# Optimization experiments

Hardware: AMD Instinct MI355X
Metric: run time of the kernel (lower is better)

The kernel has to match this reference:

```python
import jax, jax.numpy as jnp
import numpy as np

D = 1024; NHEAD = 8; NQ = 256; B = 8; HM = 64; WM = 64; S = HM * WM; FF = 4 * D
EPS_LN = 1e-5


def _ln(x, g, b):
    m = x.mean(-1, keepdims=True)
    v = ((x - m) ** 2).mean(-1, keepdims=True)
    return (x - m) / jnp.sqrt(v + EPS_LN) * g + b


def _self_attn(x, w_in, b_in, w_out, b_out, nhead):
    # x: [L, B, D] (torch MultiheadAttention, batch_first=False, eval mode)
    L, Bn, Dm = x.shape
    hd = Dm // nhead
    qkv = x @ w_in.T + b_in  # [L, B, 3D]
    q, k, v = jnp.split(qkv, 3, axis=-1)
    sp = lambda t: t.reshape(L, Bn, nhead, hd).transpose(1, 2, 0, 3)  # [B, H, L, hd]
    q, k, v = sp(q), sp(k), sp(v)
    attn = jax.nn.softmax(jnp.einsum('bhqd,bhkd->bhqk', q, k) / float(hd) ** 0.5, axis=-1)
    out = jnp.einsum('bhqk,bhkd->bhqd', attn, v)
    out = out.transpose(2, 0, 1, 3).reshape(L, Bn, Dm)
    return out @ w_out.T + b_out


def setup_inputs() -> dict:
    key = jax.random.key(0)
    ks = iter(jax.random.split(key, 40))
    nrm = lambda shape: jax.random.normal(next(ks), shape, jnp.float32) * 0.02
    return dict(
        query=jax.random.normal(next(ks), (NQ, B, D), jnp.float32),
        memory=jax.random.normal(next(ks), (S, B, D), jnp.float32),
        prev_mask=jax.random.uniform(next(ks), (B, NQ, HM, WM), dtype=jnp.float32),
        h_mem=HM, w_mem=WM,
        sa_in_w=nrm((3 * D, D)), sa_in_b=jnp.zeros((3 * D,), jnp.float32),
        sa_out_w=nrm((D, D)), sa_out_b=jnp.zeros((D,), jnp.float32),
        ln1_g=jnp.ones((D,), jnp.float32), ln1_b=jnp.zeros((D,), jnp.float32),
        ln2_g=jnp.ones((D,), jnp.float32), ln2_b=jnp.zeros((D,), jnp.float32),
        ln3_g=jnp.ones((D,), jnp.float32), ln3_b=jnp.zeros((D,), jnp.float32),
        wq=nrm((D, D)), bq=jnp.zeros((D,), jnp.float32),
        wk=nrm((D, D)), bk=jnp.zeros((D,), jnp.float32),
        wv=nrm((D, D)), bv=jnp.zeros((D,), jnp.float32),
        wo=nrm((D, D)), bo=jnp.zeros((D,), jnp.float32),
        w1=nrm((FF, D)), b1=jnp.zeros((FF,), jnp.float32),
        w2=nrm((D, FF)), b2=jnp.zeros((D,), jnp.float32),
        mask_w=nrm((S, D)), mask_b=jnp.zeros((S,), jnp.float32),
    )


def reference(query, memory, prev_mask, h_mem, w_mem,
              sa_in_w, sa_in_b, sa_out_w, sa_out_b,
              ln1_g, ln1_b, ln2_g, ln2_b, ln3_g, ln3_b,
              wq, bq, wk, bk, wv, bv, wo, bo,
              w1, b1, w2, b2, mask_w, mask_b):
    nq, Bn, d_model = query.shape
    # --- self attention block ---
    q_norm = _ln(query, ln1_g, ln1_b)
    q2 = _self_attn(q_norm, sa_in_w, sa_in_b, sa_out_w, sa_out_b, NHEAD)
    query = query + q2
    # --- masked cross attention (single-head, as in source) ---
    Q = (_ln(query, ln2_g, ln2_b) @ wq.T + bq).transpose(1, 0, 2)  # [B, NQ, D]
    K = (memory @ wk.T + bk).transpose(1, 0, 2)                    # [B, S, D]
    V = (memory @ wv.T + bv).transpose(1, 0, 2)                    # [B, S, D]
    scores = jnp.einsum('bqd,bsd->bqs', Q, K) / float(d_model) ** 0.5
    scores = scores + jnp.log(prev_mask.reshape(Bn, nq, -1) + 1e-6)
    attn = jax.nn.softmax(scores, axis=-1)
    attn_out = jnp.einsum('bqs,bsd->bqd', attn, V).transpose(1, 0, 2)  # [NQ, B, D]
    query = query + (attn_out @ wo.T + bo)
    # --- FFN ---
    h = jax.nn.gelu(_ln(query, ln3_g, ln3_b) @ w1.T + b1, approximate=False)
    query = query + (h @ w2.T + b2)
    # --- mask prediction ---
    q_for_mask = query.transpose(1, 0, 2)                # [B, NQ, D]
    mask_logits = q_for_mask @ mask_w.T + mask_b          # [B, NQ, H*W]
    pred_mask = jax.nn.sigmoid(mask_logits.reshape(Bn, nq, h_mem, w_mem))
    return (query, pred_mask)
```

## Files before the change

### kernel.cpp

```cpp
#include <hip/hip_runtime.h>
#include <cstdint>


typedef __attribute__((ext_vector_type(8))) __bf16 bf16x8;
typedef __attribute__((ext_vector_type(4))) float f32x4;
typedef __attribute__((ext_vector_type(8))) unsigned short ushort8;
typedef __attribute__((ext_vector_type(4))) unsigned short ushort4v;

__device__ __forceinline__ unsigned short f2bf(float f) {
  return __builtin_bit_cast(unsigned short, (__bf16)f);
}

__global__ __launch_bounds__(256) void cast_bf16_kernel(const float* __restrict__ in,
                                                        unsigned short* __restrict__ out,
                                                        int n8) {
  int i = blockIdx.x * 256 + threadIdx.x;
  if (i >= n8) return;
  const float4* p = (const float4*)in + (size_t)i * 2;
  float4 a = p[0], b = p[1];
  ushort8 o;
  o[0] = f2bf(a.x); o[1] = f2bf(a.y); o[2] = f2bf(a.z); o[3] = f2bf(a.w);
  o[4] = f2bf(b.x); o[5] = f2bf(b.y); o[6] = f2bf(b.z); o[7] = f2bf(b.w);
  ((ushort8*)out)[i] = o;
}

struct CastSegs {
  const float* src[9];
  int cum[10];
};
__global__ __launch_bounds__(256) void cast_multi_kernel(CastSegs cs,
                                                         unsigned short* __restrict__ out) {
  int i = blockIdx.x * 256 + threadIdx.x;
  if (i >= cs.cum[9]) return;
  int s = 0;
  while (i >= cs.cum[s + 1]) s++;
  const float4* p = (const float4*)cs.src[s] + (size_t)(i - cs.cum[s]) * 2;
  float4 a = p[0], b = p[1];
  ushort8 o;
  o[0] = f2bf(a.x); o[1] = f2bf(a.y); o[2] = f2bf(a.z); o[3] = f2bf(a.w);
  o[4] = f2bf(b.x); o[5] = f2bf(b.y); o[6] = f2bf(b.z); o[7] = f2bf(b.w);
  ((ushort8*)out)[i] = o;
}

__global__ __launch_bounds__(256) void bias_concat_kernel(const float* __restrict__ a,
                                                          const float* __restrict__ b,
                                                          float* __restrict__ o) {
  int i = blockIdx.x * 256 + threadIdx.x;
  o[i] = i < 1024 ? a[i] : b[i - 1024];
}

__global__ __launch_bounds__(256) void ln_bf16_kernel(const float* __restrict__ x,
                                                      const float* __restrict__ g,
                                                      const float* __restrict__ b,
                                                      unsigned short* __restrict__ out) {
  int row = blockIdx.x, tid = threadIdx.x;
  const float4* xr = (const float4*)(x + (size_t)row * 1024);
  float4 v = xr[tid];
  float s = v.x + v.y + v.z + v.w;
  float sq = v.x * v.x + v.y * v.y + v.z * v.z + v.w * v.w;
#pragma unroll
  for (int o = 32; o > 0; o >>= 1) { s += __shfl_xor(s, o); sq += __shfl_xor(sq, o); }
  __shared__ float red[8];
  int wave = tid >> 6, lane = tid & 63;
  if (lane == 0) { red[wave] = s; red[4 + wave] = sq; }
  __syncthreads();
  float ts = red[0] + red[1] + red[2] + red[3];
  float tq = red[4] + red[5] + red[6] + red[7];
  float mean = ts * (1.f / 1024.f);
  float var = tq * (1.f / 1024.f) - mean * mean;
  float rstd = rsqrtf(var + 1e-5f);
  float4 gv = ((const float4*)g)[tid];
  float4 bv = ((const float4*)b)[tid];
  ushort4v o;
  o[0] = f2bf((v.x - mean) * rstd * gv.x + bv.x);
  o[1] = f2bf((v.y - mean) * rstd * gv.y + bv.y);
  o[2] = f2bf((v.z - mean) * rstd * gv.z + bv.z);
  o[3] = f2bf((v.w - mean) * rstd * gv.w + bv.w);
  ((ushort4v*)(out + (size_t)row * 1024))[tid] = o;
}

template <bool MASK, int CNT>
__global__ __launch_bounds__(256) void softmax_bf16_kernel(const float* __restrict__ sc,
                                                           const float* __restrict__ pm,
                                                           unsigned short* __restrict__ out,
                                                           float scale) {
  const int L = CNT * 256;
  int row = blockIdx.x, tid = threadIdx.x;
  const float* sr = sc + (size_t)row * L;
  float vals[CNT];
  float mx = -1e30f;
#pragma unroll
  for (int i = 0; i < CNT; i++) {
    int idx = tid + (i << 8);
    float v = sr[idx] * scale;
    if (MASK) v += __logf(pm[(size_t)row * L + idx] + 1e-6f);
    vals[i] = v;
    mx = fmaxf(mx, v);
  }
#pragma unroll
  for (int o = 32; o > 0; o >>= 1) mx = fmaxf(mx, __shfl_xor(mx, o));
  __shared__ float red[8];
  int wave = tid >> 6, lane = tid & 63;
  if (lane == 0) red[wave] = mx;
  __syncthreads();
  mx = fmaxf(fmaxf(red[0], red[1]), fmaxf(red[2], red[3]));
  float sum = 0.f;
#pragma unroll
  for (int i = 0; i < CNT; i++) { vals[i] = __expf(vals[i] - mx); sum += vals[i]; }
#pragma unroll
  for (int o = 32; o > 0; o >>= 1) sum += __shfl_xor(sum, o);
  if (lane == 0) red[4 + wave] = sum;
  __syncthreads();
  float rs = 1.f / (red[4] + red[5] + red[6] + red[7]);
#pragma unroll
  for (int i = 0; i < CNT; i++)
    out[(size_t)row * L + tid + (i << 8)] = f2bf(vals[i] * rs);
}

__global__ __launch_bounds__(256) void transpose_bf16_kernel(
    const unsigned short* __restrict__ in, unsigned short* __restrict__ out,
    long in_off, int in_rs, long in_hi, long in_lo, int zdiv,
    long out_off, int out_rs, long out_hi, long out_lo) {
  __shared__ unsigned short t[32][33];
  int z = blockIdx.z;
  int zh = z / zdiv, zl = z % zdiv;
  const unsigned short* ib = in + in_off + (long)zh * in_hi + (long)zl * in_lo;
  unsigned short* ob = out + out_off + (long)zh * out_hi + (long)zl * out_lo;
  int i0 = blockIdx.x * 32;
  int j0 = blockIdx.y * 32;
  int tx = threadIdx.x & 31, ty = threadIdx.x >> 5;
#pragma unroll
  for (int r = ty; r < 32; r += 8) t[r][tx] = ib[(long)(j0 + r) * in_rs + i0 + tx];
  __syncthreads();
#pragma unroll
  for (int r = ty; r < 32; r += 8) ob[(long)(i0 + r) * out_rs + j0 + tx] = t[tx][r];
}

template <int TM, bool AF32, bool BIAS, int ACT, bool RES, bool OUTF, bool OUTB, bool KVSPLIT>
__global__ __launch_bounds__(256) void gemm_nt_kernel(
    const void* __restrict__ Av, long a_off, int lda, long a_hi, long a_lo,
    const unsigned short* __restrict__ B, long b_off, int ldb, long b_hi, long b_lo,
    const float* __restrict__ bias, const float* __restrict__ Res,
    float* __restrict__ Cf, long c_off, int ldc, long c_hi, long c_lo,
    unsigned short* __restrict__ Cb, long cb_off, int ldcb, long cb_hi, long cb_lo,
    int K, int zdiv) {
  constexpr int MI = TM / 32;
  __shared__ unsigned short As[2 * TM * 32];
  __shared__ unsigned short Bs[2 * 128 * 32];
  int tid = threadIdx.x;
  int wave = tid >> 6, lane = tid & 63;
  int z = blockIdx.z, zh = z / zdiv, zl = z % zdiv;
  long m0 = (long)blockIdx.x * TM, n0 = (long)blockIdx.y * 128;

  const unsigned short* Bb = B + b_off + zh * b_hi + zl * b_lo + n0 * ldb;
  const unsigned short* Ab16 = nullptr;
  const float* Abf = nullptr;
  if constexpr (AF32)
    Abf = (const float*)Av + a_off + zh * a_hi + zl * a_lo + m0 * lda;
  else
    Ab16 = (const unsigned short*)Av + a_off + zh * a_hi + zl * a_lo + m0 * lda;

  int srow = lane >> 2;
  int scol = (lane & 3) * 8;
  int wm = (wave >> 1) * (TM / 2), wn = (wave & 1) * 64;
  int fr = lane & 15;
  int ko = (lane >> 4) * 8;

  f32x4 acc[MI][4] = {};

  auto stage = [&](int buf, int k0) {
    unsigned short* Ad = As + buf * (TM * 32);
    unsigned short* Bd = Bs + buf * (128 * 32);
    if constexpr (AF32) {
      int row = tid >> 1;
      int cs = (tid & 1) * 16;
      const float* ap = Abf + (long)row * lda + k0 + cs;
      float4 f0 = ((const float4*)ap)[0];
      float4 f1 = ((const float4*)ap)[1];
      float4 f2 = ((const float4*)ap)[2];
      float4 f3 = ((const float4*)ap)[3];
      ushort8 u0, u1;
      u0[0] = f2bf(f0.x); u0[1] = f2bf(f0.y); u0[2] = f2bf(f0.z); u0[3] = f2bf(f0.w);
      u0[4] = f2bf(f1.x); u0[5] = f2bf(f1.y); u0[6] = f2bf(f1.z); u0[7] = f2bf(f1.w);
      u1[0] = f2bf(f2.x); u1[1] = f2bf(f2.y); u1[2] = f2bf(f2.z); u1[3] = f2bf(f2.w);
      u1[4] = f2bf(f3.x); u1[5] = f2bf(f3.y); u1[6] = f2bf(f3.z); u1[7] = f2bf(f3.w);
      ushort8* dst = (ushort8*)(Ad + row * 32 + cs);
      dst[0] = u0;
      dst[1] = u1;
    } else {
#pragma unroll
      for (int is = 0; is < TM / 64; is++) {
        int rbase = wave * (TM / 4) + is * 16;
        const unsigned short* g = Ab16 + (long)(rbase + srow) * lda + k0 + scol;
        __builtin_amdgcn_global_load_lds(
            (const __attribute__((address_space(1))) unsigned int*)g,
            (__attribute__((address_space(3))) unsigned int*)(Ad + rbase * 32), 16, 0, 0);
      }
    }
#pragma unroll
    for (int is = 0; is < 2; is++) {
      int rbase = wave * 32 + is * 16;
      const unsigned short* g = Bb + (long)(rbase + srow) * ldb + k0 + scol;
      __builtin_amdgcn_global_load_lds(
          (const __attribute__((address_space(1))) unsigned int*)g,
          (__attribute__((address_space(3))) unsigned int*)(Bd + rbase * 32), 16, 0, 0);
    }
  };

  stage(0, 0);
  int cur = 0;
  for (int k0 = 0; k0 < K; k0 += 32, cur ^= 1) {
    __syncthreads();
    if (k0 + 32 < K) stage(cur ^ 1, k0 + 32);

    const unsigned short* Ar = As + cur * (TM * 32);
    const unsigned short* Br = Bs + cur * (128 * 32);
    bf16x8 af[MI], bfv[4];
#pragma unroll
    for (int i = 0; i < MI; i++)
      af[i] = *(const bf16x8*)(Ar + (wm + i * 16 + fr) * 32 + ko);
#pragma unroll
    for (int j = 0; j < 4; j++)
      bfv[j] = *(const bf16x8*)(Br + (wn + j * 16 + fr) * 32 + ko);
#pragma unroll
    for (int i = 0; i < MI; i++)
#pragma unroll
      for (int j = 0; j < 4; j++)
        acc[i][j] = __builtin_amdgcn_mfma_f32_16x16x32_bf16(af[i], bfv[j], acc[i][j], 0, 0, 0);
  }

  long cfo = c_off + zh * c_hi + zl * c_lo;
  long cbo = cb_off + zh * cb_hi + zl * cb_lo;
  int rq = (lane >> 4) * 4;
#pragma unroll
  for (int i = 0; i < MI; i++) {
    long rbase = m0 + wm + i * 16 + rq;
#pragma unroll
    for (int j = 0; j < 4; j++) {
      long cc = n0 + wn + j * 16 + fr;
      float bsv = BIAS ? bias[cc] : 0.f;
      long p = KVSPLIT ? ((cc >> 10) * cb_hi + (cc & 1023)) : cc;
#pragma unroll
      for (int r = 0; r < 4; r++) {
        float v = acc[i][j][r] + bsv;
        long ro = rbase + r;
        if constexpr (RES) v += Res[cfo + ro * ldc + cc];
        if constexpr (ACT == 1) v = 0.5f * v * (1.f + erff(v * 0.7071067811865475f));
        if constexpr (ACT == 2) v = 1.f / (1.f + __expf(-v));
        if constexpr (OUTF) Cf[cfo + ro * ldc + cc] = v;
        if constexpr (OUTB) Cb[cbo + ro * ldcb + p] = f2bf(v);
      }
    }
  }
}

template <int TM, bool AF32, bool BIAS, int ACT, bool RES, bool OUTF, bool OUTB, bool KVSPLIT = false>
static void launch_gemm(hipStream_t s, int M, int N, int K, int nz, int zdiv,
                        const void* A, long a_off, int lda, long a_hi, long a_lo,
                        const unsigned short* B, long b_off, int ldb, long b_hi, long b_lo,
                        const float* bias, const float* Res,
                        float* Cf, long c_off, int ldc, long c_hi, long c_lo,
                        unsigned short* Cb, long cb_off, int ldcb, long cb_hi, long cb_lo) {
  dim3 g(M / TM, N / 128, nz);
  gemm_nt_kernel<TM, AF32, BIAS, ACT, RES, OUTF, OUTB, KVSPLIT><<<g, dim3(256), 0, s>>>(
      A, a_off, lda, a_hi, a_lo, B, b_off, ldb, b_hi, b_lo, bias, Res,
      Cf, c_off, ldc, c_hi, c_lo, Cb, cb_off, ldcb, cb_hi, cb_lo, K, zdiv);
}

static const long WB_SAIN = 0;
static const long WB_SAOUT = 6291456;
static const long WB_WQ = 8388608;
static const long WB_WK = 10485760;
static const long WB_WV = 12582912;
static const long WB_WO = 14680064;
static const long WB_W1 = 16777216;
static const long WB_W2 = 25165824;
static const long WB_MW = 33554432;
static const long OF_K = 41943040;
static const long OF_V = 109051904;
static const long OF_QKV = 176160768;
static const long OF_BKV = 187695104;
static const long OF_SC = 188743680;
static const long OF_P = 222298112;
static const long OF_QN = 239075328;
static const long OF_Q = 243269632;
static const long OF_CTX = 247463936;
static const long OF_MEMBF = 251658240;
static const size_t FAST_WS = 318767104;

extern "C" void kernel_launch(void* const* d_in, const int* in_sizes, int n_in,
                              void* d_out, int out_size, void* d_ws, size_t ws_size,
                              hipStream_t stream) {
  (void)in_sizes; (void)n_in; (void)out_size;
  const float* query = (const float*)d_in[0];
  const float* memoryp = (const float*)d_in[1];
  const float* prev_mask = (const float*)d_in[2];
  const float* sa_in_w = (const float*)d_in[5];
  const float* sa_in_b = (const float*)d_in[6];
  const float* sa_out_w = (const float*)d_in[7];
  const float* sa_out_b = (const float*)d_in[8];
  const float* ln1_g = (const float*)d_in[9], * ln1_b = (const float*)d_in[10];
  const float* ln2_g = (const float*)d_in[11], * ln2_b = (const float*)d_in[12];
  const float* ln3_g = (const float*)d_in[13], * ln3_b = (const float*)d_in[14];
  const float* wq = (const float*)d_in[15], * bq = (const float*)d_in[16];
  const float* wk = (const float*)d_in[17], * bk = (const float*)d_in[18];
  const float* wv = (const float*)d_in[19], * bv = (const float*)d_in[20];
  const float* wo = (const float*)d_in[21], * bo = (const float*)d_in[22];
  const float* w1 = (const float*)d_in[23], * b1 = (const float*)d_in[24];
  const float* w2 = (const float*)d_in[25], * b2 = (const float*)d_in[26];
  const float* mask_w = (const float*)d_in[27], * mask_b = (const float*)d_in[28];

  uint8_t* ws = (uint8_t*)d_ws;
  auto bf = [&](long off) { return (unsigned short*)(ws + off); };
  auto fp = [&](long off) { return (float*)(ws + off); };
  unsigned short* ZB = nullptr;
  float* ZF = nullptr;
  const bool fast = ws_size >= FAST_WS;

  {
    CastSegs cs;
    const float* srcs[9] = {sa_in_w, sa_out_w, wq, wk, wv, wo, w1, w2, mask_w};
    int n8s[9] = {393216, 131072, 131072, 131072, 131072, 131072, 524288, 524288, 524288};
    int c = 0;
    for (int i = 0; i < 9; i++) { cs.src[i] = srcs[i]; cs.cum[i] = c; c += n8s[i]; }
    cs.cum[9] = c;
    cast_multi_kernel<<<dim3((c + 255) / 256), dim3(256), 0, stream>>>(cs, bf(0));
  }

  ln_bf16_kernel<<<2048, 256, 0, stream>>>(query, ln1_g, ln1_b, bf(OF_QN));

  launch_gemm<128, false, true, 0, false, false, true>(stream, 2048, 3072, 1024, 1, 1,
      bf(OF_QN), 0, 1024, 0, 0, bf(WB_SAIN), 0, 1024, 0, 0, sa_in_b, nullptr,
      ZF, 0, 0, 0, 0, bf(OF_QKV), 0, 3072, 0, 0);

  launch_gemm<128, false, false, 0, false, true, false>(stream, 256, 256, 128, 64, 8,
      bf(OF_QKV), 0, 24576, 3072, 128,
      bf(OF_QKV), 1024, 24576, 3072, 128, nullptr, nullptr,
      fp(OF_SC), 0, 256, 524288, 65536, ZB, 0, 0, 0, 0);

  softmax_bf16_kernel<false, 1><<<16384, 256, 0, stream>>>(
      fp(OF_SC), nullptr, bf(OF_P), 0.08838834764831845f);

  transpose_bf16_kernel<<<dim3(4, 8, 64), 256, 0, stream>>>(
      bf(OF_QKV), bf(OF_QN), 2048L, 24576, 3072L, 128L, 8, 0L, 256, 262144L, 32768L);

  launch_gemm<64, false, false, 0, false, false, true>(stream, 256, 128, 256, 64, 8,
      bf(OF_P), 0, 256, 524288, 65536,
      bf(OF_QN), 0, 256, 262144, 32768, nullptr, nullptr,
      ZF, 0, 0, 0, 0, bf(OF_CTX), 0, 8192, 1024, 128);

  launch_gemm<64, false, true, 0, true, true, false>(stream, 2048, 1024, 1024, 1, 1,
      bf(OF_CTX), 0, 1024, 0, 0, bf(WB_SAOUT), 0, 1024, 0, 0, sa_out_b, query,
      fp(OF_QKV), 0, 1024, 0, 0, ZB, 0, 0, 0, 0);

  ln_bf16_kernel<<<2048, 256, 0, stream>>>(fp(OF_QKV), ln2_g, ln2_b, bf(OF_QN));

  launch_gemm<64, false, true, 0, false, false, true>(stream, 2048, 1024, 1024, 1, 1,
      bf(OF_QN), 0, 1024, 0, 0, bf(WB_WQ), 0, 1024, 0, 0, bq, nullptr,
      ZF, 0, 0, 0, 0, bf(OF_Q), 0, 1024, 0, 0);

  bias_concat_kernel<<<8, 256, 0, stream>>>(bk, bv, fp(OF_BKV));
  if (fast) {
    cast_bf16_kernel<<<16384, 256, 0, stream>>>(memoryp, bf(OF_MEMBF), 4194304);
    launch_gemm<128, false, true, 0, false, false, true, true>(stream, 32768, 2048, 1024, 1, 1,
        bf(OF_MEMBF), 0, 1024, 0, 0, bf(WB_WK), 0, 1024, 0, 0, fp(OF_BKV), nullptr,
        ZF, 0, 0, 0, 0, bf(OF_K), 0, 1024, 33554432, 0);
  } else {
    launch_gemm<128, true, true, 0, false, false, true, true>(stream, 32768, 2048, 1024, 1, 1,
        memoryp, 0, 1024, 0, 0, bf(WB_WK), 0, 1024, 0, 0, fp(OF_BKV), nullptr,
        ZF, 0, 0, 0, 0, bf(OF_K), 0, 1024, 33554432, 0);
  }

  launch_gemm<128, false, false, 0, false, true, false>(stream, 256, 4096, 1024, 8, 1,
      bf(OF_Q), 0, 8192, 1024, 0,
      bf(OF_K), 0, 8192, 1024, 0, nullptr, nullptr,
      fp(OF_SC), 0, 4096, 1048576, 0, ZB, 0, 0, 0, 0);

  softmax_bf16_kernel<true, 16><<<2048, 256, 0, stream>>>(
      fp(OF_SC), prev_mask, bf(OF_P), 0.03125f);

  transpose_bf16_kernel<<<dim3(32, 128, 8), 256, 0, stream>>>(
      bf(OF_V), bf(OF_K), 0L, 8192, 1024L, 0L, 1, 0L, 4096, 4194304L, 0L);

  launch_gemm<64, false, false, 0, false, false, true>(stream, 256, 1024, 4096, 8, 1,
      bf(OF_P), 0, 4096, 1048576, 0,
      bf(OF_K), 0, 4096, 4194304, 0, nullptr, nullptr,
      ZF, 0, 0, 0, 0, bf(OF_CTX), 0, 8192, 1024, 0);

  launch_gemm<64, false, true, 0, true, true, false>(stream, 2048, 1024, 1024, 1, 1,
      bf(OF_CTX), 0, 1024, 0, 0, bf(WB_WO), 0, 1024, 0, 0, bo, fp(OF_QKV),
      fp(OF_SC), 0, 1024, 0, 0, ZB, 0, 0, 0, 0);

  ln_bf16_kernel<<<2048, 256, 0, stream>>>(fp(OF_SC), ln3_g, ln3_b, bf(OF_QN));

  launch_gemm<128, false, true, 1, false, false, true>(stream, 2048, 4096, 1024, 1, 1,
      bf(OF_QN), 0, 1024, 0, 0, bf(WB_W1), 0, 1024, 0, 0, b1, nullptr,
      ZF, 0, 0, 0, 0, bf(OF_P), 0, 4096, 0, 0);

  launch_gemm<64, false, true, 0, true, true, true>(stream, 2048, 1024, 4096, 1, 1,
      bf(OF_P), 0, 4096, 0, 0, bf(WB_W2), 0, 4096, 0, 0, b2, fp(OF_SC),
      (float*)d_out, 0, 1024, 0, 0, bf(OF_CTX), 0, 1024, 0, 0);

  launch_gemm<128, false, true, 2, false, true, false>(stream, 256, 4096, 1024, 8, 1,
      bf(OF_CTX), 0, 8192, 1024, 0,
      bf(WB_MW), 0, 1024, 0, 0, mask_b, nullptr,
      (float*)d_out + 2097152, 0, 4096, 1048576, 0, ZB, 0, 0, 0, 0);
}
```

Baseline: 1.004 ms.

## Add dedicated 256x256-tile pipelined GEMM for K/V memory projection

Result: faster. 952.0 us (-5.2%).

```diff
diff --git a/kernel.cpp b/kernel.cpp
--- a/kernel.cpp
+++ b/kernel.cpp
@@ -250,6 +250,121 @@
         if constexpr (OUTF) Cf[cfo + ro * ldc + cc] = v;
         if constexpr (OUTB) Cb[cbo + ro * ldcb + p] = f2bf(v);
       }
+    }
+  }
+}
+
+__global__ __launch_bounds__(512, 2) void gemm256_kv_kernel(
+    const unsigned short* __restrict__ A,
+    const unsigned short* __restrict__ B,
+    const float* __restrict__ bias,
+    unsigned short* __restrict__ C,
+    long plane) {
+  __shared__ __align__(1024) unsigned short lds[4][2][8192];
+  const int K = 1024, NT = 32;
+  int tid = threadIdx.x;
+  int wave = tid >> 6, lane = tid & 63;
+  int wr = wave >> 2, wc = wave & 3;
+  int fr = lane & 15, hi = lane >> 4;
+
+  int wg = ((blockIdx.x & 7) << 7) | (blockIdx.x >> 3);
+  long m0 = (long)(wg & 127) * 256;
+  int n0 = (wg >> 7) * 256;
+
+  const unsigned short* Ab = A + m0 * K;
+  const unsigned short* Bb = B + (long)n0 * K;
+
+  int lr = lane >> 2;
+  int lc = (((lane & 3) ^ ((lane >> 5) << 1)) << 3);
+
+  auto stageA = [&](int buf, int k0) {
+    const unsigned short* g0 = Ab + (long)(wave * 16 + lr) * K + k0 + lc;
+    __builtin_amdgcn_global_load_lds(
+        (const __attribute__((address_space(1))) unsigned int*)g0,
+        (__attribute__((address_space(3))) unsigned int*)&lds[buf][0][wave * 512], 16, 0, 0);
+    const unsigned short* g1 = g0 + (long)128 * K;
+    __builtin_amdgcn_global_load_lds(
+        (const __attribute__((address_space(1))) unsigned int*)g1,
+        (__attribute__((address_space(3))) unsigned int*)&lds[buf][0][4096 + wave * 512], 16, 0, 0);
+  };
+  auto stageB = [&](int buf, int k0) {
+    const unsigned short* g0 = Bb + (long)(wave * 16 + lr) * K + k0 + lc;
+    __builtin_amdgcn_global_load_lds(
+        (const __attribute__((address_space(1))) unsigned int*)g0,
+        (__attribute__((address_space(3))) unsigned int*)&lds[buf][1][wave * 512], 16, 0, 0);
+    const unsigned short* g1 = g0 + (long)128 * K;
+    __builtin_amdgcn_global_load_lds(
+        (const __attribute__((address_space(1))) unsigned int*)g1,
+        (__attribute__((address_space(3))) unsigned int*)&lds[buf][1][4096 + wave * 512], 16, 0, 0);
+  };
+
+  int cbel = ((hi * 16) ^ ((fr >> 3) << 5)) >> 1;
+  int aoff = (wr * 128 + fr) * 32 + cbel;
+  int boff = (wc * 64 + fr) * 32 + cbel;
+
+  f32x4 acc[8][4] = {};
+
+#pragma unroll
+  for (int t = 0; t < 3; t++) { stageA(t, t * 32); stageB(t, t * 32); }
+  asm volatile("s_waitcnt vmcnt(8)" ::: "memory");
+  __builtin_amdgcn_s_barrier();
+
+#pragma unroll 4
+  for (int t = 0; t < NT; t++) {
+    int buf = t & 3;
+    const unsigned short* Abuf = &lds[buf][0][0];
+    const unsigned short* Bbuf = &lds[buf][1][0];
+    bf16x8 af[4], bfv[4];
+
+#pragma unroll
+    for (int i = 0; i < 4; i++)
+      af[i] = *(const bf16x8*)(Abuf + aoff + i * 512);
+#pragma unroll
+    for (int n = 0; n < 4; n++)
+      bfv[n] = *(const bf16x8*)(Bbuf + boff + n * 512);
+    if (t + 3 < NT) stageA((t + 3) & 3, (t + 3) * 32);
+    __builtin_amdgcn_s_barrier();
+    asm volatile("s_waitcnt lgkmcnt(0)" ::: "memory");
+    __builtin_amdgcn_sched_barrier(0);
+    __builtin_amdgcn_s_setprio(1);
+#pragma unroll
+    for (int i = 0; i < 4; i++)
+#pragma unroll
+      for (int n = 0; n < 4; n++)
+        acc[i][n] = __builtin_amdgcn_mfma_f32_16x16x32_bf16(af[i], bfv[n], acc[i][n], 0, 0, 0);
+    __builtin_amdgcn_s_setprio(0);
+    __builtin_amdgcn_s_barrier();
+
+#pragma unroll
+    for (int i = 0; i < 4; i++)
+      af[i] = *(const bf16x8*)(Abuf + aoff + 2048 + i * 512);
+    if (t + 3 < NT) stageB((t + 3) & 3, (t + 3) * 32);
+    __builtin_amdgcn_s_barrier();
+    asm volatile("s_waitcnt lgkmcnt(0)" ::: "memory");
+    __builtin_amdgcn_sched_barrier(0);
+    __builtin_amdgcn_s_setprio(1);
+#pragma unroll
+    for (int i = 0; i < 4; i++)
+#pragma unroll
+      for (int n = 0; n < 4; n++)
+        acc[4 + i][n] = __builtin_amdgcn_mfma_f32_16x16x32_bf16(af[i], bfv[n], acc[4 + i][n], 0, 0, 0);
+    __builtin_amdgcn_s_setprio(0);
+    asm volatile("s_waitcnt vmcnt(8)" ::: "memory");
+    __builtin_amdgcn_s_barrier();
+  }
+
+  int rq = hi * 4;
+#pragma unroll
+  for (int i = 0; i < 8; i++) {
+    long r0 = m0 + wr * 128 + i * 16 + rq;
+#pragma unroll
+    for (int n = 0; n < 4; n++) {
+      int cc = n0 + wc * 64 + n * 16 + fr;
+      float bsv = bias[cc];
+      long p = (long)(cc >> 10) * plane + (cc & 1023);
+#pragma unroll
+      for (int r = 0; r < 4; r++)
+        C[p + (r0 + r) * 1024] = f2bf(acc[i][n][r] + bsv);
     }
   }
 }
@@ -362,9 +477,8 @@
   bias_concat_kernel<<<8, 256, 0, stream>>>(bk, bv, fp(OF_BKV));
   if (fast) {
     cast_bf16_kernel<<<16384, 256, 0, stream>>>(memoryp, bf(OF_MEMBF), 4194304);
-    launch_gemm<128, false, true, 0, false, false, true, true>(stream, 32768, 2048, 1024, 1, 1,
-        bf(OF_MEMBF), 0, 1024, 0, 0, bf(WB_WK), 0, 1024, 0, 0, fp(OF_BKV), nullptr,
-        ZF, 0, 0, 0, 0, bf(OF_K), 0, 1024, 33554432, 0);
+    gemm256_kv_kernel<<<dim3(1024), dim3(512), 0, stream>>>(
+        bf(OF_MEMBF), bf(WB_WK), fp(OF_BKV), bf(OF_K), 33554432L);
   } else {
     launch_gemm<128, true, true, 0, false, false, true, true>(stream, 32768, 2048, 1024, 1, 1,
         memoryp, 0, 1024, 0, 0, bf(WB_WK), 0, 1024, 0, 0, fp(OF_BKV), nullptr,
```
